# Optimization experiments

Measured on AMD Instinct MI355X. Metric: run time of the kernel, lower is better.

Reference implementation:

```python
import jax, jax.numpy as jnp
import numpy as np

D_MODEL = 1024
H = 16
D_K = D_MODEL // H


def setup_inputs() -> dict:
    key = jax.random.key(0)
    ks = jax.random.split(key, 9)
    s = 0.02
    x = jax.random.normal(ks[0], (2, 2048, D_MODEL), dtype=jnp.float32)
    Wq = jax.random.normal(ks[1], (D_MODEL, D_MODEL), dtype=jnp.float32) * s
    bq = jax.random.normal(ks[2], (D_MODEL,), dtype=jnp.float32) * s
    Wk = jax.random.normal(ks[3], (D_MODEL, D_MODEL), dtype=jnp.float32) * s
    bk = jax.random.normal(ks[4], (D_MODEL,), dtype=jnp.float32) * s
    Wv = jax.random.normal(ks[5], (D_MODEL, D_MODEL), dtype=jnp.float32) * s
    bv = jax.random.normal(ks[6], (D_MODEL,), dtype=jnp.float32) * s
    Wo = jax.random.normal(ks[7], (D_MODEL, D_MODEL), dtype=jnp.float32) * s
    bo = jax.random.normal(ks[8], (D_MODEL,), dtype=jnp.float32) * s
    return {"x": x, "Wq": Wq, "bq": bq, "Wk": Wk, "bk": bk,
            "Wv": Wv, "bv": bv, "Wo": Wo, "bo": bo}


def reference(x, Wq, bq, Wk, bk, Wv, bv, Wo, bo):
    b, s, _ = x.shape
    scale = 1.0 / jnp.sqrt(jnp.float32(D_K))
    # projections; [b, s, d] -> [b, h, s, d_k]
    def split_heads(t):
        return t.reshape(b, s, H, D_K).transpose(0, 2, 1, 3)
    q = split_heads(x @ Wq + bq)
    k = split_heads(x @ Wk + bk)
    v = split_heads(x @ Wv + bv)
    scores = jnp.einsum('bhqd,bhkd->bhqk', q, k) * scale  # [b,h,s,s]
    attn = jax.nn.softmax(scores, axis=-1)
    ctx = jnp.einsum('bhqk,bhkd->bhqd', attn, v)
    ctx = ctx.transpose(0, 2, 1, 3).reshape(b, s, D_MODEL)
    return ctx @ Wo + bo + x
```

## Files before the change

### kernel.cpp

```cpp
#include <hip/hip_runtime.h>
#include <hip/hip_bf16.h>
#include <stdint.h>

#define D_MODEL 1024
#define NH 16
#define DK 64
#define S_LEN 2048

typedef __attribute__((ext_vector_type(8))) __bf16 bf16x8;
typedef __attribute__((ext_vector_type(4))) float f32x4;

#define GLOBAL_AS __attribute__((address_space(1)))
#define LDS_AS    __attribute__((address_space(3)))

__device__ __forceinline__ void async16(const ushort* g, ushort* l) {
    __builtin_amdgcn_global_load_lds(
        (const GLOBAL_AS uint32_t*)(uintptr_t)(const void*)g,
        (LDS_AS uint32_t*)(uint32_t)(uintptr_t)(void*)l,
        16, 0, 0);
}

template <int N>
__device__ __forceinline__ void pipe_barrier() {
    asm volatile("s_waitcnt vmcnt(%0)\n\ts_barrier" :: "n"(N) : "memory");
}

__device__ __forceinline__ float fast_exp2(float x) {
    float r;
    asm("v_exp_f32 %0, %1" : "=v"(r) : "v"(x));
    return r;
}

__device__ __forceinline__ ushort f2bf(float f) {
    union { float f; uint32_t u; } v; v.f = f;
    uint32_t lsb = (v.u >> 16) & 1u;
    return (ushort)((v.u + 0x7fffu + lsb) >> 16);
}

__device__ __forceinline__ uint32_t packbf(float a, float b) {
    union { float f; uint32_t u; } x, y; x.f = a; y.f = b;
    return ((x.u + 0x8000u) >> 16) | ((y.u + 0x8000u) & 0xffff0000u);
}

__device__ __forceinline__ bf16x8 ldfrag(const ushort* p) {
    union { uint4 u; bf16x8 b; } cv;
    cv.u = *(const uint4*)p;
    return cv.b;
}


__global__ void cvt_x_kernel(const float* __restrict__ x, ushort* __restrict__ xb) {
    int i = blockIdx.x * 256 + threadIdx.x;
    float4 v = ((const float4*)x)[i];
    ushort4 o;
    o.x = f2bf(v.x); o.y = f2bf(v.y); o.z = f2bf(v.z); o.w = f2bf(v.w);
    ((ushort4*)xb)[i] = o;
}

__global__ void transpose_cvt4_kernel(
    const float* __restrict__ W0, const float* __restrict__ W1,
    const float* __restrict__ W2, const float* __restrict__ W3,
    ushort* __restrict__ D0, ushort* __restrict__ D1,
    ushort* __restrict__ D2, ushort* __restrict__ D3) {
    const float* W; ushort* D;
    switch (blockIdx.z) {
        case 0: W = W0; D = D0; break;
        case 1: W = W1; D = D1; break;
        case 2: W = W2; D = D2; break;
        default: W = W3; D = D3; break;
    }
    __shared__ float tile[32][33];
    int bx = blockIdx.x * 32, by = blockIdx.y * 32;
    int tx = threadIdx.x, ty = threadIdx.y;
#pragma unroll
    for (int j = 0; j < 32; j += 8)
        tile[ty + j][tx] = W[(size_t)(by + ty + j) * D_MODEL + bx + tx];
    __syncthreads();
#pragma unroll
    for (int j = 0; j < 32; j += 8)
        D[(size_t)(bx + ty + j) * D_MODEL + by + tx] = f2bf(tile[tx][ty + j]);
}

__global__ void cvt_bias_kernel(const float* __restrict__ bq, const float* __restrict__ bk,
                                const float* __restrict__ bv, float* __restrict__ out) {
    int i = blockIdx.x * 256 + threadIdx.x;
    float v = (i < 1024) ? bq[i] : (i < 2048 ? bk[i - 1024] : bv[i - 2048]);
    out[i] = v;
}

template <int MODE>
__global__ __launch_bounds__(256) void gemm_kernel(
    const ushort* __restrict__ A, const ushort* __restrict__ Bt,
    const float* __restrict__ bias,
    ushort* __restrict__ outQ, ushort* __restrict__ outK, ushort* __restrict__ outVt,
    const float* __restrict__ xres, float* __restrict__ outF) {
    constexpr int BN = (MODE == 0) ? 128 : 64;
    constexpr int NI = (MODE == 0) ? 4 : 2;
    constexpr int NS = (MODE == 0) ? 4 : 3;
    constexpr int ABUF = 4096;
    constexpr int BBUF = (MODE == 0) ? 4096 : 2048;
    constexpr int SMEM = (MODE == 0) ? 32768 : 24576;
    __shared__ __align__(16) ushort smem[SMEM];
    ushort* sAb = smem;
    ushort* sBb = smem + 4 * ABUF;

    const int tid = threadIdx.x;
    const int wave = tid >> 6, lane = tid & 63;
    const int lr = lane & 15, lq = lane >> 4;
    const int srow = lane >> 3, sp = lane & 7;

    const int bid = blockIdx.x;
    const int xcd = bid & 7, lb = bid >> 3;
    int bx, by;
    if (MODE == 0) { bx = xcd * 3 + (lb % 3); by = lb / 3; }
    else           { by = xcd * 4 + (lb & 3); bx = lb >> 2; }
    const int blockM = by * 128;
    const int blockN = bx * BN;
    const int waveM = (wave >> 1) * 64;
    const int waveN = (MODE == 0) ? (wave & 1) * 64 : (wave & 1) * 32;

    auto stage = [&](int k0, int buf) {
        ushort* a = sAb + buf * ABUF;
#pragma unroll
        for (int t = 0; t < 2; t++) {
            int Rb = wave * 16 + t * 8;
            int R = Rb + srow;
            int L = sp ^ (R & 7);
            int m = 2 * R + (L >> 2);
            int kc = L & 3;
            async16(&A[(size_t)(blockM + m) * D_MODEL + k0 + kc * 8], a + Rb * 64);
        }
        ushort* b = sBb + buf * BBUF;
        if (MODE == 0) {
#pragma unroll
            for (int t = 0; t < 2; t++) {
                int Rb = wave * 16 + t * 8;
                int R = Rb + srow;
                int L = sp ^ (R & 7);
                int n = 2 * R + (L >> 2);
                int kc = L & 3;
                async16(&Bt[(size_t)(blockN + n) * D_MODEL + k0 + kc * 8], b + Rb * 64);
            }
        } else {
            int Rb = wave * 8;
            int R = Rb + srow;
            int L = sp ^ (R & 7);
            int n = 2 * R + (L >> 2);
            int kc = L & 3;
            async16(&Bt[(size_t)(blockN + n) * D_MODEL + k0 + kc * 8], b + Rb * 64);
        }
    };

    const int RA = (waveM >> 1) + (lr >> 1);
    const int offA = RA * 64 + ((((lr & 1) * 4 + lq) ^ (RA & 7)) * 8);
    const int RB = (waveN >> 1) + (lr >> 1);
    const int offB = RB * 64 + ((((lr & 1) * 4 + lq) ^ (RB & 7)) * 8);

    f32x4 acc[4][NI] = {};

    stage(0, 0);
    stage(32, 1);
    stage(64, 2);
    pipe_barrier<2 * NS>();

#pragma unroll 4
    for (int k = 0; k < 32; k++) {
        const int buf = k & 3;
        if (k + 3 < 32) stage((k + 3) * 32, (k + 3) & 3);
        const ushort* a = sAb + buf * ABUF;
        const ushort* b = sBb + buf * BBUF;
        bf16x8 af[4], bfr[NI];
#pragma unroll
        for (int mi = 0; mi < 4; mi++)
            af[mi] = ldfrag(&a[offA + mi * 512]);
#pragma unroll
        for (int ni = 0; ni < NI; ni++)
            bfr[ni] = ldfrag(&b[offB + ni * 512]);
#pragma unroll
        for (int mi = 0; mi < 4; mi++)
#pragma unroll
            for (int ni = 0; ni < NI; ni++)
                acc[mi][ni] = __builtin_amdgcn_mfma_f32_16x16x32_bf16(
                    af[mi], bfr[ni], acc[mi][ni], 0, 0, 0);
        if (k < 30) pipe_barrier<2 * NS>();
        else if (k == 30) pipe_barrier<0>();
    }
    __syncthreads();

    const int bglob = blockM >> 11;
    const int sbase = blockM & 2047;

    if (MODE == 0) {
        const int which = bx >> 3;
        if (which < 2) {
            const float scale = (which == 0) ? 0.1803368801f : 1.0f;
#pragma unroll
            for (int ni = 0; ni < 4; ni++) {
                const int n_loc = waveN + ni * 16 + lr;
                const float bn = bias[blockN + n_loc];
#pragma unroll
                for (int mi = 0; mi < 4; mi++)
#pragma unroll
                    for (int r = 0; r < 4; r++) {
                        int m_loc = waveM + mi * 16 + lq * 4 + r;
                        smem[m_loc * 136 + n_loc] =
                            f2bf((acc[mi][ni][r] + bn) * scale);
                    }
            }
            __syncthreads();
            ushort* outp = (which == 0) ? outQ : outK;
            const int hbase = (which == 0) ? bx * 2 : (bx - 8) * 2;
#pragma unroll
            for (int j = 0; j < 8; j++) {
                int c = tid + j * 256;
                int m = c >> 4, nc = c & 15;
                int hh = nc >> 3, d8 = nc & 7;
                uint4 w = *(uint4*)&smem[m * 136 + nc * 8];
                size_t bh = (size_t)(bglob * NH + hbase + hh);
                *(uint4*)&outp[(bh * S_LEN + sbase + m) * DK + d8 * 8] = w;
            }
        } else {
#pragma unroll
            for (int ni = 0; ni < 4; ni++) {
                const int n_loc = waveN + ni * 16 + lr;
                const float bn = bias[blockN + n_loc];
#pragma unroll
                for (int mi = 0; mi < 4; mi++) {
                    uint2 w;
                    w.x = packbf(acc[mi][ni][0] + bn, acc[mi][ni][1] + bn);
                    w.y = packbf(acc[mi][ni][2] + bn, acc[mi][ni][3] + bn);
                    int m_base = waveM + mi * 16 + lq * 4;
                    *(uint2*)&smem[n_loc * 136 + m_base] = w;
                }
            }
            __syncthreads();
            const int hbase = (bx - 16) * 2;
#pragma unroll
            for (int j = 0; j < 8; j++) {
                int c = tid + j * 256;
                int n_loc = c >> 4, m8 = c & 15;
                int d = n_loc & 63, hh = n_loc >> 6;
                uint4 w = *(uint4*)&smem[n_loc * 136 + m8 * 8];
                size_t bh = (size_t)(bglob * NH + hbase + hh);
                *(uint4*)&outVt[(bh * DK + d) * S_LEN + sbase + m8 * 8] = w;
            }
        }
    } else {
        float* sCf = (float*)smem;
#pragma unroll
        for (int ni = 0; ni < 2; ni++) {
            const int n_loc = waveN + ni * 16 + lr;
            const float bn = bias[blockN + n_loc];
#pragma unroll
            for (int mi = 0; mi < 4; mi++)
#pragma unroll
                for (int r = 0; r < 4; r++) {
                    int m_loc = waveM + mi * 16 + lq * 4 + r;
                    sCf[m_loc * 68 + n_loc] = acc[mi][ni][r] + bn;
                }
        }
        __syncthreads();
#pragma unroll
        for (int j = 0; j < 8; j++) {
            int c = tid + j * 256;
            int m = c >> 4, nc = c & 15;
            float4 v = *(float4*)&sCf[m * 68 + nc * 4];
            size_t idx = (size_t)(blockM + m) * D_MODEL + blockN + nc * 4;
            float4 xr = *(const float4*)&xres[idx];
            v.x += xr.x; v.y += xr.y; v.z += xr.z; v.w += xr.w;
            *(float4*)&outF[idx] = v;
        }
    }
}

__global__ __launch_bounds__(256, 2) void attn_kernel(
    const ushort* __restrict__ Q, const ushort* __restrict__ Km,
    const ushort* __restrict__ Vt, ushort* __restrict__ ctx) {
    const int bid = blockIdx.x;
    const int xcd = bid & 7, lb = bid >> 3;
    const int bh = xcd * 4 + (lb & 3);
    const int qt = lb >> 2;
    const int q0 = qt * 128;
    __shared__ __align__(16) ushort sK[3][64 * 64];
    __shared__ __align__(16) ushort sV[3][64 * 64];
    __shared__ __align__(16) ushort sQP[4][32 * 64];
    const int tid = threadIdx.x;
    const int wave = tid >> 6, lane = tid & 63;
    const int lr = lane & 15, lq = lane >> 4;
    const int srow = lane >> 3, sp = lane & 7;
    const ushort* Qh = Q + (size_t)bh * S_LEN * DK;
    const ushort* Kh = Km + (size_t)bh * S_LEN * DK;
    const ushort* Vh = Vt + (size_t)bh * DK * S_LEN;
    ushort* sPw = sQP[wave];

#pragma unroll
    for (int t = 0; t < 4; t++) {
        int row = t * 8 + srow;
        int c = sp ^ (row & 7);
        async16(&Qh[(size_t)(q0 + wave * 32 + row) * DK + c * 8],
                &sPw[t * 8 * 64]);
    }

    auto stageKV = [&](int k0, int buf) {
#pragma unroll
        for (int t = 0; t < 2; t++) {
            int row = wave * 16 + t * 8 + srow;
            int c = sp ^ (row & 7);
            async16(&Kh[(size_t)(k0 + row) * DK + c * 8],
                    &sK[buf][(wave * 16 + t * 8) * 64]);
            async16(&Vh[(size_t)row * S_LEN + k0 + c * 8],
                    &sV[buf][(wave * 16 + t * 8) * 64]);
        }
    };

    stageKV(0, 0);
    stageKV(64, 1);
    __syncthreads();

    bf16x8 qf[2][2];
#pragma unroll
    for (int nj = 0; nj < 2; nj++)
#pragma unroll
        for (int kk = 0; kk < 2; kk++)
            qf[nj][kk] = ldfrag(&sPw[(nj * 16 + lr) * 64 +
                                     (((kk * 4 + lq) ^ (lr & 7)) * 8)]);

    union { uint4 u; bf16x8 b; } one_u;
    one_u.u = make_uint4(0x3F803F80u, 0x3F803F80u, 0x3F803F80u, 0x3F803F80u);
    const bf16x8 ones = one_u.b;

    f32x4 cacc[2][4] = {};
    f32x4 ssum[2] = {};

    int cur = 0;
    for (int k = 0; k < 32; k++) {
        int nx = cur + 2; if (nx >= 3) nx -= 3;
        if (k + 2 < 32) stageKV((k + 2) * 64, nx);
        const ushort* sk = sK[cur];
        const ushort* sv = sV[cur];

        f32x4 sacc[4][2] = {};
#pragma unroll
        for (int kk = 0; kk < 2; kk++) {
            bf16x8 kf[4];
            int swz = ((kk * 4 + lq) ^ (lr & 7)) * 8;
#pragma unroll
            for (int mi = 0; mi < 4; mi++)
                kf[mi] = ldfrag(&sk[(mi * 16 + lr) * 64 + swz]);
#pragma unroll
            for (int mi = 0; mi < 4; mi++)
#pragma unroll
                for (int nj = 0; nj < 2; nj++)
                    sacc[mi][nj] = __builtin_amdgcn_mfma_f32_16x16x32_bf16(
                        kf[mi], qf[nj][kk], sacc[mi][nj], 0, 0, 0);
        }

#pragma unroll
        for (int mi = 0; mi < 4; mi++)
#pragma unroll
            for (int nj = 0; nj < 2; nj++) {
                float p0 = fast_exp2(sacc[mi][nj][0]);
                float p1 = fast_exp2(sacc[mi][nj][1]);
                float p2 = fast_exp2(sacc[mi][nj][2]);
                float p3 = fast_exp2(sacc[mi][nj][3]);
                uint2 w;
                w.x = packbf(p0, p1);
                w.y = packbf(p2, p3);
                int physc = (mi * 2 + (lq >> 1)) ^ (lr & 7);
                *(uint2*)&sPw[(nj * 16 + lr) * 64 + physc * 8 + (lq & 1) * 4] = w;
            }

#pragma unroll
        for (int ks = 0; ks < 2; ks++) {
            bf16x8 pf[2], vf[4];
            int swz = ((ks * 4 + lq) ^ (lr & 7)) * 8;
#pragma unroll
            for (int nj = 0; nj < 2; nj++)
                pf[nj] = ldfrag(&sPw[(nj * 16 + lr) * 64 + swz]);
#pragma unroll
            for (int nd = 0; nd < 4; nd++)
                vf[nd] = ldfrag(&sv[(nd * 16 + lr) * 64 + swz]);
#pragma unroll
            for (int nj = 0; nj < 2; nj++)
#pragma unroll
                for (int nd = 0; nd < 4; nd++)
                    cacc[nj][nd] = __builtin_amdgcn_mfma_f32_16x16x32_bf16(
                        pf[nj], vf[nd], cacc[nj][nd], 0, 0, 0);
#pragma unroll
            for (int nj = 0; nj < 2; nj++)
                ssum[nj] = __builtin_amdgcn_mfma_f32_16x16x32_bf16(
                    pf[nj], ones, ssum[nj], 0, 0, 0);
        }

        if (k < 30) pipe_barrier<4>();
        else if (k == 30) pipe_barrier<0>();
        cur = (cur == 2) ? 0 : cur + 1;
    }

    const int b = bh >> 4, h = bh & 15;
    float inv[2][4];
#pragma unroll
    for (int nj = 0; nj < 2; nj++)
#pragma unroll
        for (int r = 0; r < 4; r++)
            inv[nj][r] = __builtin_amdgcn_rcpf(ssum[nj][r]);
#pragma unroll
    for (int nj = 0; nj < 2; nj++)
#pragma unroll
        for (int nd = 0; nd < 4; nd++)
#pragma unroll
            for (int r = 0; r < 4; r++) {
                int qrow = q0 + wave * 32 + nj * 16 + lq * 4 + r;
                int d = nd * 16 + lr;
                float v = cacc[nj][nd][r] * inv[nj][r];
                ctx[(size_t)(b * S_LEN + qrow) * D_MODEL + h * DK + d] = f2bf(v);
            }
}


extern "C" void kernel_launch(void* const* d_in, const int* in_sizes, int n_in,
                              void* d_out, int out_size, void* d_ws, size_t ws_size,
                              hipStream_t stream) {
    const float* x  = (const float*)d_in[0];
    const float* Wq = (const float*)d_in[1];
    const float* bq = (const float*)d_in[2];
    const float* Wk = (const float*)d_in[3];
    const float* bk = (const float*)d_in[4];
    const float* Wv = (const float*)d_in[5];
    const float* bv = (const float*)d_in[6];
    const float* Wo = (const float*)d_in[7];
    const float* bo = (const float*)d_in[8];

    char* ws = (char*)d_ws;
    ushort* xb    = (ushort*)(ws);
    ushort* wqkv  = (ushort*)(ws + (8ull  << 20));
    ushort* wo_t  = (ushort*)(ws + (14ull << 20));
    ushort* qbuf  = (ushort*)(ws + (16ull << 20));
    ushort* kbuf  = (ushort*)(ws + (24ull << 20));
    ushort* vtb   = (ushort*)(ws + (32ull << 20));
    ushort* ctx   = (ushort*)(ws + (40ull << 20));
    float*  biasq = (float*)(ws + (48ull << 20));

    cvt_x_kernel<<<4096, 256, 0, stream>>>(x, xb);
    transpose_cvt4_kernel<<<dim3(32, 32, 4), dim3(32, 8), 0, stream>>>(
        Wq, Wk, Wv, Wo, wqkv, wqkv + 1024 * 1024, wqkv + 2 * 1024 * 1024, wo_t);
    cvt_bias_kernel<<<12, 256, 0, stream>>>(bq, bk, bv, biasq);

    gemm_kernel<0><<<768, 256, 0, stream>>>(
        xb, wqkv, biasq, qbuf, kbuf, vtb, nullptr, nullptr);
    attn_kernel<<<512, 256, 0, stream>>>(qbuf, kbuf, vtb, ctx);
    gemm_kernel<1><<<512, 256, 0, stream>>>(
        ctx, wo_t, bo, nullptr, nullptr, nullptr, x, (float*)d_out);
}
```

Measured before the change: 207.7 us.

## Split attention work across eight waves with 16 query rows each

The attention kernel now runs 512 threads (8 waves) per block, with each wave owning 16 query rows instead of 32. K/V staging is split across the eight waves. The aim is more waves for latency hiding and less register pressure, at the cost of each wave reusing its K/V fragment loads over fewer MFMAs. It also adds s_setprio around the MFMA groups and switches the P packing to a round-to-nearest bf16 conversion intrinsic.

```diff
diff --git a/kernel.cpp b/kernel.cpp
--- a/kernel.cpp
+++ b/kernel.cpp
@@ -40,6 +40,12 @@
 __device__ __forceinline__ uint32_t packbf(float a, float b) {
     union { float f; uint32_t u; } x, y; x.f = a; y.f = b;
     return ((x.u + 0x8000u) >> 16) | ((y.u + 0x8000u) & 0xffff0000u);
+}
+
+__device__ __forceinline__ uint32_t packbf_rn(float a, float b) {
+    union { __hip_bfloat162 h; uint32_t u; } cv;
+    cv.h = __float22bfloat162_rn(make_float2(a, b));
+    return cv.u;
 }
 
 __device__ __forceinline__ bf16x8 ldfrag(const ushort* p) {
@@ -273,7 +279,7 @@
     }
 }
 
-__global__ __launch_bounds__(256, 2) void attn_kernel(
+__global__ __launch_bounds__(512, 4) void attn_kernel(
     const ushort* __restrict__ Q, const ushort* __restrict__ Km,
     const ushort* __restrict__ Vt, ushort* __restrict__ ctx) {
     const int bid = blockIdx.x;
@@ -283,7 +289,7 @@
     const int q0 = qt * 128;
     __shared__ __align__(16) ushort sK[3][64 * 64];
     __shared__ __align__(16) ushort sV[3][64 * 64];
-    __shared__ __align__(16) ushort sQP[4][32 * 64];
+    __shared__ __align__(16) ushort sQP[8][16 * 64];
     const int tid = threadIdx.x;
     const int wave = tid >> 6, lane = tid & 63;
     const int lr = lane & 15, lq = lane >> 4;
@@ -294,43 +300,37 @@
     ushort* sPw = sQP[wave];
 
 #pragma unroll
-    for (int t = 0; t < 4; t++) {
+    for (int t = 0; t < 2; t++) {
         int row = t * 8 + srow;
         int c = sp ^ (row & 7);
-        async16(&Qh[(size_t)(q0 + wave * 32 + row) * DK + c * 8],
+        async16(&Qh[(size_t)(q0 + wave * 16 + row) * DK + c * 8],
                 &sPw[t * 8 * 64]);
     }
 
     auto stageKV = [&](int k0, int buf) {
-#pragma unroll
-        for (int t = 0; t < 2; t++) {
-            int row = wave * 16 + t * 8 + srow;
-            int c = sp ^ (row & 7);
-            async16(&Kh[(size_t)(k0 + row) * DK + c * 8],
-                    &sK[buf][(wave * 16 + t * 8) * 64]);
-            async16(&Vh[(size_t)row * S_LEN + k0 + c * 8],
-                    &sV[buf][(wave * 16 + t * 8) * 64]);
-        }
+        int row = wave * 8 + srow;
+        int c = sp ^ (row & 7);
+        async16(&Kh[(size_t)(k0 + row) * DK + c * 8],
+                &sK[buf][wave * 8 * 64]);
+        async16(&Vh[(size_t)row * S_LEN + k0 + c * 8],
+                &sV[buf][wave * 8 * 64]);
     };
 
     stageKV(0, 0);
     stageKV(64, 1);
     __syncthreads();
 
-    bf16x8 qf[2][2];
-#pragma unroll
-    for (int nj = 0; nj < 2; nj++)
-#pragma unroll
-        for (int kk = 0; kk < 2; kk++)
-            qf[nj][kk] = ldfrag(&sPw[(nj * 16 + lr) * 64 +
-                                     (((kk * 4 + lq) ^ (lr & 7)) * 8)]);
+    bf16x8 qf[2];
+#pragma unroll
+    for (int kk = 0; kk < 2; kk++)
+        qf[kk] = ldfrag(&sPw[lr * 64 + (((kk * 4 + lq) ^ (lr & 7)) * 8)]);
 
     union { uint4 u; bf16x8 b; } one_u;
     one_u.u = make_uint4(0x3F803F80u, 0x3F803F80u, 0x3F803F80u, 0x3F803F80u);
     const bf16x8 ones = one_u.b;
 
-    f32x4 cacc[2][4] = {};
-    f32x4 ssum[2] = {};
+    f32x4 cacc[4] = {};
+    f32x4 ssum = {};
 
     int cur = 0;
     for (int k = 0; k < 32; k++) {
@@ -339,7 +339,7 @@
         const ushort* sk = sK[cur];
         const ushort* sv = sV[cur];
 
-        f32x4 sacc[4][2] = {};
+        f32x4 sacc[4] = {};
 #pragma unroll
         for (int kk = 0; kk < 2; kk++) {
             bf16x8 kf[4];
@@ -347,74 +347,64 @@
 #pragma unroll
             for (int mi = 0; mi < 4; mi++)
                 kf[mi] = ldfrag(&sk[(mi * 16 + lr) * 64 + swz]);
+            __builtin_amdgcn_s_setprio(1);
 #pragma unroll
             for (int mi = 0; mi < 4; mi++)
-#pragma unroll
-                for (int nj = 0; nj < 2; nj++)
-                    sacc[mi][nj] = __builtin_amdgcn_mfma_f32_16x16x32_bf16(
-                        kf[mi], qf[nj][kk], sacc[mi][nj], 0, 0, 0);
-        }
-
-#pragma unroll
-        for (int mi = 0; mi < 4; mi++)
-#pragma unroll
-            for (int nj = 0; nj < 2; nj++) {
-                float p0 = fast_exp2(sacc[mi][nj][0]);
-                float p1 = fast_exp2(sacc[mi][nj][1]);
-                float p2 = fast_exp2(sacc[mi][nj][2]);
-                float p3 = fast_exp2(sacc[mi][nj][3]);
-                uint2 w;
-                w.x = packbf(p0, p1);
-                w.y = packbf(p2, p3);
-                int physc = (mi * 2 + (lq >> 1)) ^ (lr & 7);
-                *(uint2*)&sPw[(nj * 16 + lr) * 64 + physc * 8 + (lq & 1) * 4] = w;
-            }
+                sacc[mi] = __builtin_amdgcn_mfma_f32_16x16x32_bf16(
+                    kf[mi], qf[kk], sacc[mi], 0, 0, 0);
+            __builtin_amdgcn_s_setprio(0);
+        }
+
+#pragma unroll
+        for (int mi = 0; mi < 4; mi++) {
+            float p0 = fast_exp2(sacc[mi][0]);
+            float p1 = fast_exp2(sacc[mi][1]);
+            float p2 = fast_exp2(sacc[mi][2]);
+            float p3 = fast_exp2(sacc[mi][3]);
+            uint2 w;
+            w.x = packbf_rn(p0, p1);
+            w.y = packbf_rn(p2, p3);
+            int physc = (mi * 2 + (lq >> 1)) ^ (lr & 7);
+            *(uint2*)&sPw[lr * 64 + physc * 8 + (lq & 1) * 4] = w;
+        }
 
 #pragma unroll
         for (int ks = 0; ks < 2; ks++) {
-            bf16x8 pf[2], vf[4];
+            bf16x8 pf, vf[4];
             int swz = ((ks * 4 + lq) ^ (lr & 7)) * 8;
-#pragma unroll
-            for (int nj = 0; nj < 2; nj++)
-                pf[nj] = ldfrag(&sPw[(nj * 16 + lr) * 64 + swz]);
+            pf = ldfrag(&sPw[lr * 64 + swz]);
 #pragma unroll
             for (int nd = 0; nd < 4; nd++)
                 vf[nd] = ldfrag(&sv[(nd * 16 + lr) * 64 + swz]);
-#pragma unroll
-            for (int nj = 0; nj < 2; nj++)
-#pragma unroll
-                for (int nd = 0; nd < 4; nd++)
-                    cacc[nj][nd] = __builtin_amdgcn_mfma_f32_16x16x32_bf16(
-                        pf[nj], vf[nd], cacc[nj][nd], 0, 0, 0);
-#pragma unroll
-            for (int nj = 0; nj < 2; nj++)
-                ssum[nj] = __builtin_amdgcn_mfma_f32_16x16x32_bf16(
-                    pf[nj], ones, ssum[nj], 0, 0, 0);
-        }
-
-        if (k < 30) pipe_barrier<4>();
+            __builtin_amdgcn_s_setprio(1);
+#pragma unroll
+            for (int nd = 0; nd < 4; nd++)
+                cacc[nd] = __builtin_amdgcn_mfma_f32_16x16x32_bf16(
+                    pf, vf[nd], cacc[nd], 0, 0, 0);
+            ssum = __builtin_amdgcn_mfma_f32_16x16x32_bf16(
+                pf, ones, ssum, 0, 0, 0);
+            __builtin_amdgcn_s_setprio(0);
+        }
+
+        if (k < 30) pipe_barrier<2>();
         else if (k == 30) pipe_barrier<0>();
         cur = (cur == 2) ? 0 : cur + 1;
     }
 
     const int b = bh >> 4, h = bh & 15;
-    float inv[2][4];
-#pragma unroll
-    for (int nj = 0; nj < 2; nj++)
-#pragma unroll
-        for (int r = 0; r < 4; r++)
-            inv[nj][r] = __builtin_amdgcn_rcpf(ssum[nj][r]);
-#pragma unroll
-    for (int nj = 0; nj < 2; nj++)
-#pragma unroll
-        for (int nd = 0; nd < 4; nd++)
-#pragma unroll
-            for (int r = 0; r < 4; r++) {
-                int qrow = q0 + wave * 32 + nj * 16 + lq * 4 + r;
-                int d = nd * 16 + lr;
-                float v = cacc[nj][nd][r] * inv[nj][r];
-                ctx[(size_t)(b * S_LEN + qrow) * D_MODEL + h * DK + d] = f2bf(v);
-            }
+    float inv[4];
+#pragma unroll
+    for (int r = 0; r < 4; r++)
+        inv[r] = __builtin_amdgcn_rcpf(ssum[r]);
+#pragma unroll
+    for (int nd = 0; nd < 4; nd++)
+#pragma unroll
+        for (int r = 0; r < 4; r++) {
+            int qrow = q0 + wave * 16 + lq * 4 + r;
+            int d = nd * 16 + lr;
+            float v = cacc[nd][r] * inv[r];
+            ctx[(size_t)(b * S_LEN + qrow) * D_MODEL + h * DK + d] = f2bf(v);
+        }
 }
 
 
@@ -448,7 +438,7 @@
 
     gemm_kernel<0><<<768, 256, 0, stream>>>(
         xb, wqkv, biasq, qbuf, kbuf, vtb, nullptr, nullptr);
-    attn_kernel<<<512, 256, 0, stream>>>(qbuf, kbuf, vtb, ctx);
+    attn_kernel<<<512, 512, 0, stream>>>(qbuf, kbuf, vtb, ctx);
     gemm_kernel<1><<<512, 256, 0, stream>>>(
         ctx, wo_t, bo, nullptr, nullptr, nullptr, x, (float*)d_out);
 }
```

After: 204.6 us. Within noise of the previous version (-1.5%).

## Software-pipeline attention QK with PV and trim GEMM stages for occupancy

Applied to the files above, without the earlier changes.

The attention loop is restructured so the QK^T MFMAs for the next key tile run alongside the PV MFMAs for the current tile, with exp/pack of P moved after the barrier. s_setprio is raised around the MFMA blocks. The projection GEMMs drop from a 4-buffer to a 3-buffer LDS pipeline and request 3 blocks per CU through launch bounds, trading prefetch depth for occupancy. P packing switches to the library round-to-nearest bf16 conversion. The attention barrier now waits for all outstanding loads each iteration, which may expose more load latency.

```diff
diff --git a/kernel.cpp b/kernel.cpp
--- a/kernel.cpp
+++ b/kernel.cpp
@@ -40,6 +40,12 @@
 __device__ __forceinline__ uint32_t packbf(float a, float b) {
     union { float f; uint32_t u; } x, y; x.f = a; y.f = b;
     return ((x.u + 0x8000u) >> 16) | ((y.u + 0x8000u) & 0xffff0000u);
+}
+
+__device__ __forceinline__ uint32_t packbf_rn(float a, float b) {
+    union { __hip_bfloat162 h; uint32_t u; } cv;
+    cv.h = __float22bfloat162_rn(make_float2(a, b));
+    return cv.u;
 }
 
 __device__ __forceinline__ bf16x8 ldfrag(const ushort* p) {
@@ -89,7 +95,7 @@
 }
 
 template <int MODE>
-__global__ __launch_bounds__(256) void gemm_kernel(
+__global__ __launch_bounds__(256, 3) void gemm_kernel(
     const ushort* __restrict__ A, const ushort* __restrict__ Bt,
     const float* __restrict__ bias,
     ushort* __restrict__ outQ, ushort* __restrict__ outK, ushort* __restrict__ outVt,
@@ -99,10 +105,10 @@
     constexpr int NS = (MODE == 0) ? 4 : 3;
     constexpr int ABUF = 4096;
     constexpr int BBUF = (MODE == 0) ? 4096 : 2048;
-    constexpr int SMEM = (MODE == 0) ? 32768 : 24576;
+    constexpr int SMEM = (MODE == 0) ? 24576 : 18432;
     __shared__ __align__(16) ushort smem[SMEM];
     ushort* sAb = smem;
-    ushort* sBb = smem + 4 * ABUF;
+    ushort* sBb = smem + 3 * ABUF;
 
     const int tid = threadIdx.x;
     const int wave = tid >> 6, lane = tid & 63;
@@ -160,13 +166,12 @@
 
     stage(0, 0);
     stage(32, 1);
-    stage(64, 2);
-    pipe_barrier<2 * NS>();
-
-#pragma unroll 4
+    pipe_barrier<NS>();
+
+#pragma unroll
     for (int k = 0; k < 32; k++) {
-        const int buf = k & 3;
-        if (k + 3 < 32) stage((k + 3) * 32, (k + 3) & 3);
+        const int buf = k % 3;
+        if (k + 2 < 32) stage((k + 2) * 32, (k + 2) % 3);
         const ushort* a = sAb + buf * ABUF;
         const ushort* b = sBb + buf * BBUF;
         bf16x8 af[4], bfr[NI];
@@ -182,7 +187,7 @@
             for (int ni = 0; ni < NI; ni++)
                 acc[mi][ni] = __builtin_amdgcn_mfma_f32_16x16x32_bf16(
                     af[mi], bfr[ni], acc[mi][ni], 0, 0, 0);
-        if (k < 30) pipe_barrier<2 * NS>();
+        if (k < 30) pipe_barrier<NS>();
         else if (k == 30) pipe_barrier<0>();
     }
     __syncthreads();
@@ -332,14 +337,7 @@
     f32x4 cacc[2][4] = {};
     f32x4 ssum[2] = {};
 
-    int cur = 0;
-    for (int k = 0; k < 32; k++) {
-        int nx = cur + 2; if (nx >= 3) nx -= 3;
-        if (k + 2 < 32) stageKV((k + 2) * 64, nx);
-        const ushort* sk = sK[cur];
-        const ushort* sv = sV[cur];
-
-        f32x4 sacc[4][2] = {};
+    auto qk = [&](const ushort* sk, f32x4 (*sacc)[2]) {
 #pragma unroll
         for (int kk = 0; kk < 2; kk++) {
             bf16x8 kf[4];
@@ -347,14 +345,18 @@
 #pragma unroll
             for (int mi = 0; mi < 4; mi++)
                 kf[mi] = ldfrag(&sk[(mi * 16 + lr) * 64 + swz]);
+            __builtin_amdgcn_s_setprio(1);
 #pragma unroll
             for (int mi = 0; mi < 4; mi++)
 #pragma unroll
                 for (int nj = 0; nj < 2; nj++)
                     sacc[mi][nj] = __builtin_amdgcn_mfma_f32_16x16x32_bf16(
                         kf[mi], qf[nj][kk], sacc[mi][nj], 0, 0, 0);
-        }
-
+            __builtin_amdgcn_s_setprio(0);
+        }
+    };
+
+    auto expP = [&](f32x4 (*sacc)[2]) {
 #pragma unroll
         for (int mi = 0; mi < 4; mi++)
 #pragma unroll
@@ -364,12 +366,14 @@
                 float p2 = fast_exp2(sacc[mi][nj][2]);
                 float p3 = fast_exp2(sacc[mi][nj][3]);
                 uint2 w;
-                w.x = packbf(p0, p1);
-                w.y = packbf(p2, p3);
+                w.x = packbf_rn(p0, p1);
+                w.y = packbf_rn(p2, p3);
                 int physc = (mi * 2 + (lq >> 1)) ^ (lr & 7);
                 *(uint2*)&sPw[(nj * 16 + lr) * 64 + physc * 8 + (lq & 1) * 4] = w;
             }
-
+    };
+
+    auto pv = [&](const ushort* sv) {
 #pragma unroll
         for (int ks = 0; ks < 2; ks++) {
             bf16x8 pf[2], vf[4];
@@ -380,6 +384,7 @@
 #pragma unroll
             for (int nd = 0; nd < 4; nd++)
                 vf[nd] = ldfrag(&sv[(nd * 16 + lr) * 64 + swz]);
+            __builtin_amdgcn_s_setprio(1);
 #pragma unroll
             for (int nj = 0; nj < 2; nj++)
 #pragma unroll
@@ -390,12 +395,27 @@
             for (int nj = 0; nj < 2; nj++)
                 ssum[nj] = __builtin_amdgcn_mfma_f32_16x16x32_bf16(
                     pf[nj], ones, ssum[nj], 0, 0, 0);
-        }
-
-        if (k < 30) pipe_barrier<4>();
-        else if (k == 30) pipe_barrier<0>();
-        cur = (cur == 2) ? 0 : cur + 1;
-    }
+            __builtin_amdgcn_s_setprio(0);
+        }
+    };
+
+    {
+        f32x4 s0[4][2] = {};
+        qk(sK[0], s0);
+        expP(s0);
+    }
+
+    int c0 = 0, c1 = 1, c2 = 2;
+    for (int k = 0; k < 31; k++) {
+        if (k < 30) stageKV((k + 2) * 64, c2);
+        f32x4 s2[4][2] = {};
+        qk(sK[c1], s2);
+        pv(sV[c0]);
+        pipe_barrier<0>();
+        expP(s2);
+        int t = c0; c0 = c1; c1 = c2; c2 = t;
+    }
+    pv(sV[c0]);
 
     const int b = bh >> 4, h = bh & 15;
     float inv[2][4];
```

New measurement: 193.4 us. -6.9%, faster.
